# Optimization experiments

Hardware: AMD Instinct MI355X
Metric: run time of the kernel (lower is better)

Reference implementation:

```python
import jax, jax.numpy as jnp
import numpy as np

B, N, D, H = 4, 2048, 1024, 16
DH = D // H


def setup_inputs() -> dict:
    key = jax.random.key(0)
    ks = jax.random.split(key, 9)
    std = 0.02
    return {
        "x": jax.random.normal(ks[0], (B, N, D), dtype=jnp.float32),
        "Wq": jax.random.normal(ks[1], (D, D), dtype=jnp.float32) * std,
        "bq": jnp.zeros((D,), dtype=jnp.float32),
        "Wk": jax.random.normal(ks[2], (D, D), dtype=jnp.float32) * std,
        "bk": jnp.zeros((D,), dtype=jnp.float32),
        "Wv": jax.random.normal(ks[3], (D, D), dtype=jnp.float32) * std,
        "bv": jnp.zeros((D,), dtype=jnp.float32),
        "Wo": jax.random.normal(ks[4], (D, D), dtype=jnp.float32) * std,
        "bo": jnp.zeros((D,), dtype=jnp.float32),
        "k": 8,
        "dilation": 2,
    }


def _dilated_mask(n_q, n_k, k, dilation):
    # allowed[i, j] = True iff |j - i| <= k*dilation and (j - i) % dilation == 0
    i = jnp.arange(n_q)[:, None]
    j = jnp.arange(n_k)[None, :]
    d = j - i
    return (jnp.abs(d) <= k * dilation) & ((d % dilation) == 0)


def reference(x, Wq, bq, Wk, bk, Wv, bv, Wo, bo, k, dilation):
    b, n_q, d_model = x.shape
    n_heads = H
    d_head = d_model // n_heads
    # self-attention: context = x
    q = (x @ Wq + bq).reshape(b, n_q, n_heads, d_head).transpose(0, 2, 1, 3)  # (B,H,Nq,Dh)
    kk = (x @ Wk + bk).reshape(b, n_q, n_heads, d_head).transpose(0, 2, 1, 3)
    v = (x @ Wv + bv).reshape(b, n_q, n_heads, d_head).transpose(0, 2, 1, 3)

    scale = 1.0 / np.sqrt(d_head).astype(np.float32)
    scores = jnp.einsum("bhqd,bhkd->bhqk", q, kk) * scale  # (B,H,Nq,Nk)
    allowed = _dilated_mask(n_q, n_q, k, dilation)  # (Nq,Nk)
    scores = jnp.where(allowed[None, None], scores, -jnp.inf)
    attn = jax.nn.softmax(scores, axis=-1)
    out = jnp.einsum("bhqk,bhkd->bhqd", attn, v)  # (B,H,Nq,Dh)
    out = out.transpose(0, 2, 1, 3).reshape(b, n_q, d_model)
    return out @ Wo + bo
```

## Files before the change

### kernel.cpp

```cpp
#include <hip/hip_runtime.h>
#include <hip/hip_bf16.h>
#include <hip/hip_fp16.h>
#include <stdint.h>

using bf16 = __hip_bfloat16;

typedef __bf16    bf16x8 __attribute__((ext_vector_type(8)));
typedef float     floatx4 __attribute__((ext_vector_type(4)));
typedef _Float16  f16x2 __attribute__((ext_vector_type(2)));
typedef _Float16  f16x8 __attribute__((ext_vector_type(8)));

typedef __attribute__((address_space(3))) void as3_void;
typedef __attribute__((address_space(1))) void as1_void;

#define GLD_LDS16(gp, lp) \
  __builtin_amdgcn_global_load_lds((as1_void*)(uintptr_t)(gp), (as3_void*)(uintptr_t)(lp), 16, 0, 0)

#if __has_builtin(__builtin_amdgcn_fdot2)
#define DOT2(a, b, c) __builtin_amdgcn_fdot2((a), (b), (c), false)
#else
#define DOT2(a, b, c) ((c) + (float)(a)[0] * (float)(b)[0] + (float)(a)[1] * (float)(b)[1])
#endif

__global__ __launch_bounds__(256) void prep_kernel(
    const float* __restrict__ x,
    const float* __restrict__ Wq, const float* __restrict__ Wk,
    const float* __restrict__ Wv, const float* __restrict__ Wo,
    bf16* __restrict__ xbf, bf16* __restrict__ WTqkv, bf16* __restrict__ WoT) {
  __shared__ float tile[64 * 68];
  const int blk = blockIdx.x;
  const int tid = threadIdx.x;
  if (blk < 1024) {
    const int z = blk >> 8, t = blk & 255;
    const float* src = (z == 0) ? Wq : (z == 1) ? Wk : (z == 2) ? Wv : Wo;
    bf16* dst = (z < 3) ? (WTqkv + (size_t)z * 1024 * 1024) : WoT;
    const int nbase = (t & 15) * 64, kbase = (t >> 4) * 64;
    const int r1 = tid >> 4, c1 = tid & 15;
#pragma unroll
    for (int it = 0; it < 4; ++it) {
      const int row = r1 + it * 16;
      const float4 v = *(const float4*)(src + (size_t)(kbase + row) * 1024 + nbase + c1 * 4);
      *(float4*)(tile + row * 68 + c1 * 4) = v;
    }
    __syncthreads();
    const int c2 = tid & 7, n2 = tid >> 3;
#pragma unroll
    for (int it2 = 0; it2 < 2; ++it2) {
      const int n = n2 + it2 * 32;
      bf16 o[8];
#pragma unroll
      for (int s = 0; s < 8; ++s) o[s] = (bf16)tile[(8 * c2 + s) * 68 + n];
      *(uint4*)(dst + (size_t)(nbase + n) * 1024 + kbase + 8 * c2) = *(const uint4*)o;
    }
  } else {
    const size_t basei = ((size_t)(blk - 1024) * 256 + tid) * 16;
#pragma unroll
    for (int h = 0; h < 2; ++h) {
      const float4 a = *(const float4*)(x + basei + h * 8);
      const float4 b = *(const float4*)(x + basei + h * 8 + 4);
      bf16 o[8] = {(bf16)a.x, (bf16)a.y, (bf16)a.z, (bf16)a.w,
                   (bf16)b.x, (bf16)b.y, (bf16)b.z, (bf16)b.w};
      *(uint4*)(xbf + basei + h * 8) = *(const uint4*)o;
    }
  }
}

template <int MODE>
__global__ __launch_bounds__(256) void gemm_bt_kernel(
    const bf16* __restrict__ A, const bf16* __restrict__ Bt,
    const float* __restrict__ b0, const float* __restrict__ b1, const float* __restrict__ b2,
    __half* __restrict__ out0, __half* __restrict__ out1, __half* __restrict__ out2,
    float* __restrict__ fout) {
  const int tid  = threadIdx.x;
  const int m0   = blockIdx.x * 128;
  const int n0   = blockIdx.y * 128;
  const int lane = tid & 63;
  const int wave = tid >> 6;
  const int wr   = (wave >> 1) * 64;
  const int wc   = (wave & 1) * 64;
  const int quad = lane >> 4;
  const int l16  = lane & 15;

  __shared__ alignas(16) bf16 As[128 * 64];
  __shared__ alignas(16) bf16 Bs[128 * 64];

  const int srow = tid >> 3;
  const int cg   = (tid & 7) ^ (srow & 7);
  uint64_t aoff;
  if (MODE == 0) {
    aoff = (uint64_t)(m0 + srow) * 1024 + cg * 8;
  } else {
    const int b = m0 >> 11, seq0 = m0 & 2047;
    aoff = (uint64_t)b * 2097152 + (uint64_t)(seq0 + srow) * 64 + cg * 8;
  }
  const uint64_t boff = (uint64_t)(n0 + srow) * 1024 + cg * 8;

  floatx4 acc[4][4];
#pragma unroll
  for (int i = 0; i < 4; ++i)
#pragma unroll
    for (int j = 0; j < 4; ++j) {
      floatx4 z = {0.f, 0.f, 0.f, 0.f};
      acc[i][j] = z;
    }

  for (int k0 = 0; k0 < 1024; k0 += 64) {
    __syncthreads();
#pragma unroll
    for (int it = 0; it < 4; ++it) {
      if (MODE == 0)
        GLD_LDS16(A + aoff + (uint64_t)it * 32768 + k0, (char*)As + it * 4096 + tid * 16);
      else
        GLD_LDS16(A + aoff + (uint64_t)it * 2048 + (uint64_t)(k0 >> 6) * 131072,
                  (char*)As + it * 4096 + tid * 16);
      GLD_LDS16(Bt + boff + (uint64_t)it * 32768 + k0, (char*)Bs + it * 4096 + tid * 16);
    }
    __syncthreads();

#pragma unroll
    for (int kc = 0; kc < 2; ++kc) {
      bf16x8 af[4], bfr[4];
#pragma unroll
      for (int i = 0; i < 4; ++i) {
        const int mrow = wr + i * 16 + l16;
        const int pca  = (kc * 4 + quad) ^ (mrow & 7);
        af[i] = *(const bf16x8*)(As + mrow * 64 + pca * 8);
        const int nrow = wc + i * 16 + l16;
        const int pcb  = (kc * 4 + quad) ^ (nrow & 7);
        bfr[i] = *(const bf16x8*)(Bs + nrow * 64 + pcb * 8);
      }
#pragma unroll
      for (int i = 0; i < 4; ++i)
#pragma unroll
        for (int j = 0; j < 4; ++j)
          acc[i][j] = __builtin_amdgcn_mfma_f32_16x16x32_bf16(af[i], bfr[j], acc[i][j], 0, 0, 0);
    }
  }

#pragma unroll
  for (int i = 0; i < 4; ++i) {
#pragma unroll
    for (int j = 0; j < 4; ++j) {
#pragma unroll
      for (int r = 0; r < 4; ++r) {
        const int m = m0 + wr + i * 16 + quad * 4 + r;
        const int n = n0 + wc + j * 16 + l16;
        float v = acc[i][j][r];
        if (MODE == 0) {
          const int which = n >> 10;
          const int c = n & 1023;
          const float* bp = (which == 0) ? b0 : (which == 1) ? b1 : b2;
          __half* op      = (which == 0) ? out0 : (which == 1) ? out1 : out2;
          v += bp[c];
          const int h = c >> 6, dh = c & 63;
          const int bb = m >> 11, seq = m & 2047;
          op[(uint64_t)(bb * 16 + h) * 131072 + (uint64_t)seq * 64 + dh] = (__half)v;
        } else {
          fout[(uint64_t)m * 1024 + n] = v + b0[n];
        }
      }
    }
  }
}

#define RMAX 32

#define ATTN_T_CORE(KEXPR, VEXPR)                                          \
  {                                                                        \
    f16x8 kc[8], vc[8];                                                    \
    _Pragma("unroll")                                                      \
    for (int c = 0; c < 8; ++c) {                                          \
      kc[c] = *(const f16x8*)(KEXPR);                                      \
      vc[c] = *(const f16x8*)(VEXPR);                                      \
    }                                                                      \
    float sp[4] = {0.f, 0.f, 0.f, 0.f};                                    \
    _Pragma("unroll")                                                      \
    for (int c = 0; c < 8; ++c) {                                          \
      _Pragma("unroll")                                                    \
      for (int u = 0; u < 4; ++u) {                                        \
        const f16x2 qa = {q[c][2 * u], q[c][2 * u + 1]};                   \
        const f16x2 ka = {kc[c][2 * u], kc[c][2 * u + 1]};                 \
        sp[c & 3] = DOT2(qa, ka, sp[c & 3]);                               \
      }                                                                    \
    }                                                                      \
    const float s = (sp[0] + sp[1]) + (sp[2] + sp[3]);                     \
    const float pe = valid ? __expf(s * 0.125f) : 0.f;                     \
    l += pe;                                                               \
    const _Float16 ph = (_Float16)pe;                                      \
    const f16x2 pe2 = {ph, ph};                                            \
    _Pragma("unroll")                                                      \
    for (int c = 0; c < 8; ++c) {                                          \
      _Pragma("unroll")                                                    \
      for (int u = 0; u < 4; ++u) {                                        \
        const f16x2 va = {vc[c][2 * u], vc[c][2 * u + 1]};                 \
        oo[c * 4 + u] += pe2 * va;                                         \
      }                                                                    \
    }                                                                      \
  }

__global__ __launch_bounds__(256) void dilated_attn_kernel(
    const __half* __restrict__ Q, const __half* __restrict__ K, const __half* __restrict__ V,
    bf16* __restrict__ attn_out, const int* __restrict__ kptr, const int* __restrict__ dptr) {
  const int tid = threadIdx.x;
  const int bh  = blockIdx.x >> 3;
  const int qb  = blockIdx.x & 7;
  const int Q0  = qb * 256;
  const int kk  = kptr[0];
  const int dil = dptr[0];
  const int R   = kk * dil;

  const size_t base = (size_t)bh * 2048 * 64;

  __shared__ alignas(16) _Float16 Ks[320 * 64];
  __shared__ alignas(16) _Float16 Vs[320 * 64];

  const int jlo_b = (Q0 - RMAX > 0) ? Q0 - RMAX : 0;
  const int jhi_b = (Q0 + 255 + RMAX < 2047) ? Q0 + 255 + RMAX : 2047;
  const int nrows = jhi_b - jlo_b + 1;
  const bool fast = (R <= RMAX) && (dil > 0);

  if (fast) {
    for (int c = tid; c < nrows * 8; c += 256) {
      const int r = c >> 3, ch = c & 7;
      const int slot = ch ^ (r & 7);
      const size_t g = base + (size_t)(jlo_b + r) * 64 + ch * 8;
      *(f16x8*)(Ks + r * 64 + slot * 8) = *(const f16x8*)((const _Float16*)K + g);
      *(f16x8*)(Vs + r * 64 + slot * 8) = *(const f16x8*)((const _Float16*)V + g);
    }
    __syncthreads();
  }

  const int wave = tid >> 6, lane = tid & 63;
  const int i = Q0 + wave * 64 + lane;

  f16x8 q[8];
#pragma unroll
  for (int t = 0; t < 8; ++t)
    q[t] = *(const f16x8*)((const _Float16*)Q + base + (size_t)i * 64 + t * 8);

  float l = 0.f;
  f16x2 oo[32];
#pragma unroll
  for (int t = 0; t < 32; ++t) oo[t] = (f16x2){(_Float16)0, (_Float16)0};

  if (fast) {
    const int rbase = i - jlo_b;
    for (int t = -kk; t <= kk; ++t) {
      const int j = i + t * dil;
      const bool valid = (unsigned)j < 2048u;
      int row = rbase + t * dil;
      row = (row < 0) ? 0 : (row >= nrows ? nrows - 1 : row);
      const int ro = row * 64, rx = row & 7;
      ATTN_T_CORE(Ks + ro + ((c ^ rx) << 3), Vs + ro + ((c ^ rx) << 3))
    }
  } else {
    for (int t = -kk; t <= kk; ++t) {
      const int j = i + t * dil;
      const bool valid = (unsigned)j < 2048u;
      const size_t go = base + (size_t)(valid ? j : i) * 64;
      ATTN_T_CORE((const _Float16*)K + go + c * 8, (const _Float16*)V + go + c * 8)
    }
  }

  const float linv = 1.f / fmaxf(l, 1e-30f);
  alignas(16) bf16 orow[64];
#pragma unroll
  for (int t = 0; t < 32; ++t) {
    orow[2 * t]     = (bf16)((float)oo[t][0] * linv);
    orow[2 * t + 1] = (bf16)((float)oo[t][1] * linv);
  }
  bf16* dst = attn_out + base + (size_t)i * 64;
#pragma unroll
  for (int c = 0; c < 8; ++c)
    *(uint4*)(dst + c * 8) = *(const uint4*)(orow + c * 8);
}

extern "C" void kernel_launch(void* const* d_in, const int* in_sizes, int n_in,
                              void* d_out, int out_size, void* d_ws, size_t ws_size,
                              hipStream_t stream) {
  const float* x  = (const float*)d_in[0];
  const float* Wq = (const float*)d_in[1];
  const float* bq = (const float*)d_in[2];
  const float* Wk = (const float*)d_in[3];
  const float* bk = (const float*)d_in[4];
  const float* Wv = (const float*)d_in[5];
  const float* bv = (const float*)d_in[6];
  const float* Wo = (const float*)d_in[7];
  const float* bo = (const float*)d_in[8];
  const int* kp   = (const int*)d_in[9];
  const int* dp   = (const int*)d_in[10];
  float* out = (float*)d_out;

  bf16*   xbf   = (bf16*)d_ws;
  bf16*   WTqkv = xbf + 8388608;
  bf16*   WoT   = WTqkv + 3072 * 1024;
  __half* qbuf  = (__half*)(WoT + 1024 * 1024);
  __half* kbuf  = qbuf + 8388608;
  __half* vbuf  = kbuf + 8388608;
  bf16*   attnH = xbf;

  prep_kernel<<<dim3(3072), 256, 0, stream>>>(x, Wq, Wk, Wv, Wo, xbf, WTqkv, WoT);

  gemm_bt_kernel<0><<<dim3(64, 24), 256, 0, stream>>>(xbf, WTqkv, bq, bk, bv,
                                                      qbuf, kbuf, vbuf, nullptr);

  dilated_attn_kernel<<<dim3(512), 256, 0, stream>>>(qbuf, kbuf, vbuf, attnH, kp, dp);

  gemm_bt_kernel<1><<<dim3(64, 8), 256, 0, stream>>>(attnH, WoT, bo, nullptr, nullptr,
                                                     nullptr, nullptr, nullptr, out);
}
```

Before: 208.3 us.

## Rewrite dilated attention with MFMA banded tiles and transposed V in LDS

Replaces the per-thread scalar dot2 attention loop with an MFMA-based version. Each wave computes 16 queries against a 16-wide key band using mfma 16x16x32 f16, writes exp-probabilities to LDS, and multiplies by a transposed V tile held in LDS. Blocks shrink to 64 queries, so the grid grows to 2048. The dense band computes many masked-out entries when dilation > 1, and the V transpose scatter-store plus zero-fill add LDS traffic. The fallback path is serialized to 64 threads.

```diff
diff --git a/kernel.cpp b/kernel.cpp
--- a/kernel.cpp
+++ b/kernel.cpp
@@ -163,116 +163,144 @@
   }
 }
 
-#define RMAX 32
-
-#define ATTN_T_CORE(KEXPR, VEXPR)                                          \
-  {                                                                        \
-    f16x8 kc[8], vc[8];                                                    \
-    _Pragma("unroll")                                                      \
-    for (int c = 0; c < 8; ++c) {                                          \
-      kc[c] = *(const f16x8*)(KEXPR);                                      \
-      vc[c] = *(const f16x8*)(VEXPR);                                      \
-    }                                                                      \
-    float sp[4] = {0.f, 0.f, 0.f, 0.f};                                    \
-    _Pragma("unroll")                                                      \
-    for (int c = 0; c < 8; ++c) {                                          \
-      _Pragma("unroll")                                                    \
-      for (int u = 0; u < 4; ++u) {                                        \
-        const f16x2 qa = {q[c][2 * u], q[c][2 * u + 1]};                   \
-        const f16x2 ka = {kc[c][2 * u], kc[c][2 * u + 1]};                 \
-        sp[c & 3] = DOT2(qa, ka, sp[c & 3]);                               \
-      }                                                                    \
-    }                                                                      \
-    const float s = (sp[0] + sp[1]) + (sp[2] + sp[3]);                     \
-    const float pe = valid ? __expf(s * 0.125f) : 0.f;                     \
-    l += pe;                                                               \
-    const _Float16 ph = (_Float16)pe;                                      \
-    const f16x2 pe2 = {ph, ph};                                            \
-    _Pragma("unroll")                                                      \
-    for (int c = 0; c < 8; ++c) {                                          \
-      _Pragma("unroll")                                                    \
-      for (int u = 0; u < 4; ++u) {                                        \
-        const f16x2 va = {vc[c][2 * u], vc[c][2 * u + 1]};                 \
-        oo[c * 4 + u] += pe2 * va;                                         \
-      }                                                                    \
-    }                                                                      \
-  }
-
-__global__ __launch_bounds__(256) void dilated_attn_kernel(
+#define RMAXA 32
+#define VTS 176
+#define PS  104
+
+__global__ __launch_bounds__(256) void dilated_attn_mfma_kernel(
     const __half* __restrict__ Q, const __half* __restrict__ K, const __half* __restrict__ V,
     bf16* __restrict__ attn_out, const int* __restrict__ kptr, const int* __restrict__ dptr) {
-  const int tid = threadIdx.x;
-  const int bh  = blockIdx.x >> 3;
-  const int qb  = blockIdx.x & 7;
-  const int Q0  = qb * 256;
+  const int tid  = threadIdx.x;
+  const int wave = tid >> 6, lane = tid & 63;
+  const int quad = lane >> 4, l16 = lane & 15;
+  const int bh = blockIdx.x >> 5;
+  const int Q0 = (blockIdx.x & 31) * 64;
   const int kk  = kptr[0];
   const int dil = dptr[0];
   const int R   = kk * dil;
-
   const size_t base = (size_t)bh * 2048 * 64;
-
-  __shared__ alignas(16) _Float16 Ks[320 * 64];
-  __shared__ alignas(16) _Float16 Vs[320 * 64];
-
-  const int jlo_b = (Q0 - RMAX > 0) ? Q0 - RMAX : 0;
-  const int jhi_b = (Q0 + 255 + RMAX < 2047) ? Q0 + 255 + RMAX : 2047;
-  const int nrows = jhi_b - jlo_b + 1;
-  const bool fast = (R <= RMAX) && (dil > 0);
+  const _Float16* Qh = (const _Float16*)Q;
+  const _Float16* Kh = (const _Float16*)K;
+  const _Float16* Vh = (const _Float16*)V;
+
+  __shared__ alignas(16) _Float16 smem[64 * VTS + 4 * 16 * PS];
+  _Float16* VT = smem;
+  _Float16* Pw = smem + 64 * VTS + wave * 16 * PS;
+
+  const bool fast = (R <= RMAXA) && (dil >= 1);
 
   if (fast) {
-    for (int c = tid; c < nrows * 8; c += 256) {
-      const int r = c >> 3, ch = c & 7;
-      const int slot = ch ^ (r & 7);
-      const size_t g = base + (size_t)(jlo_b + r) * 64 + ch * 8;
-      *(f16x8*)(Ks + r * 64 + slot * 8) = *(const f16x8*)((const _Float16*)K + g);
-      *(f16x8*)(Vs + r * 64 + slot * 8) = *(const f16x8*)((const _Float16*)V + g);
-    }
-    __syncthreads();
-  }
-
-  const int wave = tid >> 6, lane = tid & 63;
-  const int i = Q0 + wave * 64 + lane;
-
-  f16x8 q[8];
-#pragma unroll
-  for (int t = 0; t < 8; ++t)
-    q[t] = *(const f16x8*)((const _Float16*)Q + base + (size_t)i * 64 + t * 8);
-
-  float l = 0.f;
-  f16x2 oo[32];
-#pragma unroll
-  for (int t = 0; t < 32; ++t) oo[t] = (f16x2){(_Float16)0, (_Float16)0};
-
-  if (fast) {
-    const int rbase = i - jlo_b;
+    {
+      const int nch = (64 * VTS + 4 * 16 * PS) / 8;
+      const f16x8 z = {0, 0, 0, 0, 0, 0, 0, 0};
+      for (int c = tid; c < nch; c += 256) ((f16x8*)smem)[c] = z;
+    }
+    __syncthreads();
+
+    const int jlo = Q0 - R;
+    const int lo = (jlo > 0) ? jlo : 0;
+    const int hi = (Q0 + 63 + R < 2047) ? Q0 + 63 + R : 2047;
+    const int nrows = hi - lo + 1;
+    for (int idx = tid; idx < nrows * 8; idx += 256) {
+      const int r = idx >> 3, c = idx & 7;
+      const int j = lo + r;
+      const f16x8 v = *(const f16x8*)(Vh + base + (size_t)j * 64 + c * 8);
+      const int col = j - jlo + 32;
+#pragma unroll
+      for (int s = 0; s < 8; ++s) VT[(c * 8 + s) * VTS + col] = v[s];
+    }
+    __syncthreads();
+
+    const int i0 = Q0 + wave * 16;
+    const f16x8 a0 = *(const f16x8*)(Qh + base + (size_t)(i0 + l16) * 64 + quad * 8);
+    const f16x8 a1 = *(const f16x8*)(Qh + base + (size_t)(i0 + l16) * 64 + 32 + quad * 8);
+
+    const int nkt = (16 + 2 * R + 15) >> 4;
+    const int jw0 = i0 - R;
+    float lsum[4] = {0.f, 0.f, 0.f, 0.f};
+    const floatx4 zf = {0.f, 0.f, 0.f, 0.f};
+
+    for (int kt = 0; kt < nkt; ++kt) {
+      const int j0 = jw0 + 16 * kt;
+      const int jn = j0 + l16;
+      const int jc = (jn < 0) ? 0 : (jn > 2047 ? 2047 : jn);
+      const f16x8 b0 = *(const f16x8*)(Kh + base + (size_t)jc * 64 + quad * 8);
+      const f16x8 b1 = *(const f16x8*)(Kh + base + (size_t)jc * 64 + 32 + quad * 8);
+      floatx4 s4 = __builtin_amdgcn_mfma_f32_16x16x32_f16(a0, b0, zf, 0, 0, 0);
+      s4 = __builtin_amdgcn_mfma_f32_16x16x32_f16(a1, b1, s4, 0, 0, 0);
+#pragma unroll
+      for (int r = 0; r < 4; ++r) {
+        const int m = quad * 4 + r;
+        const int d = jn - (i0 + m);
+        const bool valid = ((unsigned)jn < 2048u) && (d >= -R) && (d <= R) && (d % dil == 0);
+        const float pe = valid ? __expf(s4[r] * 0.125f) : 0.f;
+        lsum[r] += pe;
+        Pw[m * PS + kt * 16 + l16] = (_Float16)pe;
+      }
+    }
+#pragma unroll
+    for (int r = 0; r < 4; ++r) {
+      lsum[r] += __shfl_xor(lsum[r], 1);
+      lsum[r] += __shfl_xor(lsum[r], 2);
+      lsum[r] += __shfl_xor(lsum[r], 4);
+      lsum[r] += __shfl_xor(lsum[r], 8);
+    }
+
+    const int nkc = (nkt * 16 + 31) >> 5;
+    floatx4 o[4] = {zf, zf, zf, zf};
+    const int vbase = 16 * wave + 32;
+    for (int c = 0; c < nkc; ++c) {
+      const f16x8 pa = *(const f16x8*)(Pw + l16 * PS + c * 32 + quad * 8);
+#pragma unroll
+      for (int t = 0; t < 4; ++t) {
+        const f16x8 vb = *(const f16x8*)(VT + (t * 16 + l16) * VTS + vbase + c * 32 + quad * 8);
+        o[t] = __builtin_amdgcn_mfma_f32_16x16x32_f16(pa, vb, o[t], 0, 0, 0);
+      }
+    }
+
+#pragma unroll
+    for (int t = 0; t < 4; ++t) {
+#pragma unroll
+      for (int r = 0; r < 4; ++r)
+        Pw[(quad * 4 + r) * PS + t * 16 + l16] = (_Float16)(o[t][r] / lsum[r]);
+    }
+    const int orow = lane >> 2, oseg = lane & 3;
+#pragma unroll
+    for (int hseg = 0; hseg < 2; ++hseg) {
+      const f16x8 ov = *(const f16x8*)(Pw + orow * PS + oseg * 16 + hseg * 8);
+      bf16 ob[8];
+#pragma unroll
+      for (int s = 0; s < 8; ++s) ob[s] = (bf16)(float)ov[s];
+      *(uint4*)(attn_out + base + (size_t)(i0 + orow) * 64 + oseg * 16 + hseg * 8) =
+          *(const uint4*)ob;
+    }
+    return;
+  }
+
+  {
+    const int i = Q0 + (tid >> 2);
+  }
+  if (tid < 64) {
+    const int i = Q0 + tid;
+    float l = 0.f;
+    float oacc[64];
+#pragma unroll
+    for (int u = 0; u < 64; ++u) oacc[u] = 0.f;
+    float qv[64];
+#pragma unroll
+    for (int u = 0; u < 64; ++u) qv[u] = (float)Qh[base + (size_t)i * 64 + u];
     for (int t = -kk; t <= kk; ++t) {
-      const int j = i + t * dil;
-      const bool valid = (unsigned)j < 2048u;
-      int row = rbase + t * dil;
-      row = (row < 0) ? 0 : (row >= nrows ? nrows - 1 : row);
-      const int ro = row * 64, rx = row & 7;
-      ATTN_T_CORE(Ks + ro + ((c ^ rx) << 3), Vs + ro + ((c ^ rx) << 3))
-    }
-  } else {
-    for (int t = -kk; t <= kk; ++t) {
-      const int j = i + t * dil;
-      const bool valid = (unsigned)j < 2048u;
-      const size_t go = base + (size_t)(valid ? j : i) * 64;
-      ATTN_T_CORE((const _Float16*)K + go + c * 8, (const _Float16*)V + go + c * 8)
-    }
-  }
-
-  const float linv = 1.f / fmaxf(l, 1e-30f);
-  alignas(16) bf16 orow[64];
-#pragma unroll
-  for (int t = 0; t < 32; ++t) {
-    orow[2 * t]     = (bf16)((float)oo[t][0] * linv);
-    orow[2 * t + 1] = (bf16)((float)oo[t][1] * linv);
-  }
-  bf16* dst = attn_out + base + (size_t)i * 64;
-#pragma unroll
-  for (int c = 0; c < 8; ++c)
-    *(uint4*)(dst + c * 8) = *(const uint4*)(orow + c * 8);
+      const int j = i + (int)((long long)t * dil);
+      if (j < 0 || j >= 2048) continue;
+      float s = 0.f;
+      for (int u = 0; u < 64; ++u) s += qv[u] * (float)Kh[base + (size_t)j * 64 + u];
+      const float pe = __expf(s * 0.125f);
+      l += pe;
+      for (int u = 0; u < 64; ++u) oacc[u] += pe * (float)Vh[base + (size_t)j * 64 + u];
+    }
+    for (int u = 0; u < 64; ++u)
+      attn_out[base + (size_t)i * 64 + u] = (bf16)(oacc[u] / l);
+  }
 }
 
 extern "C" void kernel_launch(void* const* d_in, const int* in_sizes, int n_in,
@@ -304,7 +332,7 @@
   gemm_bt_kernel<0><<<dim3(64, 24), 256, 0, stream>>>(xbf, WTqkv, bq, bk, bv,
                                                       qbuf, kbuf, vbuf, nullptr);
 
-  dilated_attn_kernel<<<dim3(512), 256, 0, stream>>>(qbuf, kbuf, vbuf, attnH, kp, dp);
+  dilated_attn_mfma_kernel<<<dim3(2048), 256, 0, stream>>>(qbuf, kbuf, vbuf, attnH, kp, dp);
 
   gemm_bt_kernel<1><<<dim3(64, 8), 256, 0, stream>>>(attnH, WoT, bo, nullptr, nullptr,
                                                      nullptr, nullptr, nullptr, out);
```

Measured after the change: 207.9 us. About the same (-0.2%).
